# Kernel tuning notes

Measured on AMD Instinct MI355X. Metric: run time of the kernel, lower is better.

## Reference

```python
import jax, jax.numpy as jnp
import numpy as np

NEG_BIG = -9e15
ALPHA = 0.2  # leakyrelu negative slope

N, F_IN, F_OUT = 8192, 512, 64


def setup_inputs() -> dict:
    key = jax.random.key(0)
    k1, k2, k3, k4 = jax.random.split(key, 4)
    input = jax.random.normal(k1, (N, F_IN), dtype=jnp.float32)
    adj = jax.random.randint(k2, (N, N), 0, 2, dtype=jnp.int32)
    W = jax.random.normal(k3, (F_IN, F_OUT), dtype=jnp.float32) * 0.05
    a = jax.random.normal(k4, (2 * F_OUT, 1), dtype=jnp.float32) * 0.1
    return {"input": input, "adj": adj, "W": W, "a": a}


def reference(input, adj, W, a):
    # h: [N, F_out]
    h = input @ W
    # The original builds a_input[i,j] = concat(h_i, h_j) and dots with a.
    # Decompose: e_ij = leakyrelu(h_i @ a_src + h_j @ a_dst) -- identical math,
    # avoids the N*N*2F intermediate.
    a_src = a[:F_OUT, 0]  # [F_out]
    a_dst = a[F_OUT:, 0]  # [F_out]
    s_src = h @ a_src     # [N]
    s_dst = h @ a_dst     # [N]
    e = jax.nn.leaky_relu(s_src[:, None] + s_dst[None, :], negative_slope=ALPHA)  # [N, N]
    masked = jnp.where(adj > 0, e, jnp.float32(NEG_BIG))
    attention = jax.nn.softmax(masked, axis=1)  # dropout omitted (eval mode)
    h_prime = attention @ h  # [N, F_out]
    return jax.nn.elu(h_prime)  # concat=True
```

## Files before the change

kernel.cpp:

```cpp
#include <hip/hip_runtime.h>
#include <hip/hip_bf16.h>

namespace {
constexpr int kN    = 8192;
constexpr int kFin  = 512;
constexpr int kFout = 64;
constexpr float kAlpha = 0.2f;
constexpr int kJSplit = 4;
constexpr int kJLen   = kN / kJSplit;
constexpr int kChunks = kJLen / 128;

using bf16x8 = __attribute__((ext_vector_type(8))) short;
using f32x4  = __attribute__((ext_vector_type(4))) float;

__device__ __forceinline__ unsigned short f2bf(float x) {
  return __builtin_bit_cast(unsigned short, __float2bfloat16(x));
}
__device__ __forceinline__ float lrelu(float x) {
  return fmaxf(x, kAlpha * x);
}
__device__ __forceinline__ unsigned int fkey(float x) {
  unsigned int b = __float_as_uint(x);
  return (b & 0x80000000u) ? ~b : (b | 0x80000000u);
}
__device__ __forceinline__ float fdec(unsigned int k) {
  return (k & 0x80000000u) ? __uint_as_float(k ^ 0x80000000u) : __uint_as_float(~k);
}
}

__global__ __launch_bounds__(256) void k_prep(
    const int* __restrict__ adj, const float* __restrict__ X,
    const float* __restrict__ W, const float* __restrict__ A,
    unsigned long long* __restrict__ mask, unsigned short* __restrict__ hTf,
    float* __restrict__ s_src, float* __restrict__ s_dst,
    unsigned int* __restrict__ Smax_u)
{
  const int t = threadIdx.x;
  const int wv = t >> 6, lane = t & 63;

  if (blockIdx.x >= 512) {
    const int mwave = (blockIdx.x - 512) * 4 + wv;
    constexpr int kMaskWaves = 2048 * 4;
    const int4* __restrict__ a4 = (const int4*)adj;
    const int grp = lane >> 4;
    const unsigned long long shft = 4ull * (lane & 15);
#pragma unroll 2
    for (int it = 0; it < 32; ++it) {
      const size_t base4 = ((size_t)it * kMaskWaves + mwave) * 64;
      const int4 v = a4[base4 + lane];
      const unsigned int nib = (v.x > 0 ? 1u : 0u) | (v.y > 0 ? 2u : 0u) |
                               (v.z > 0 ? 4u : 0u) | (v.w > 0 ? 8u : 0u);
      unsigned long long val = (unsigned long long)nib << shft;
      val |= __shfl_xor(val, 1, 64);
      val |= __shfl_xor(val, 2, 64);
      val |= __shfl_xor(val, 4, 64);
      val |= __shfl_xor(val, 8, 64);
      if ((lane & 15) == 0) {
        const size_t baseInt = base4 * 4;
        const size_t row = baseInt >> 13;
        const size_t jw  = (baseInt & 8191) >> 6;
        mask[row * 128 + jw + grp] = val;
      }
    }
    return;
  }

  const int wvu = __builtin_amdgcn_readfirstlane(wv);
  const int f = lane;
  const int i0 = blockIdx.x * 16;
  const int r0l = wvu * 4;

  __shared__ unsigned short h_sm[16][64];
  __shared__ float red[4];

  const float* x0 = X + (size_t)(i0 + r0l) * kFin;
  float acc0 = 0.f, acc1 = 0.f, acc2 = 0.f, acc3 = 0.f;
#pragma unroll 2
  for (int k = 0; k < kFin; k += 4) {
    const float4 xa = *(const float4*)(x0 + k);
    const float4 xb = *(const float4*)(x0 + kFin + k);
    const float4 xc = *(const float4*)(x0 + 2 * kFin + k);
    const float4 xd = *(const float4*)(x0 + 3 * kFin + k);
#pragma unroll
    for (int j = 0; j < 4; ++j) {
      const float wk = W[(k + j) * kFout + f];
      acc0 = fmaf(((const float*)&xa)[j], wk, acc0);
      acc1 = fmaf(((const float*)&xb)[j], wk, acc1);
      acc2 = fmaf(((const float*)&xc)[j], wk, acc2);
      acc3 = fmaf(((const float*)&xd)[j], wk, acc3);
    }
  }

  const float asrc = A[f], adst = A[kFout + f];
  float accs[4] = {acc0, acc1, acc2, acc3};
  float dmax = -3.4e38f;
#pragma unroll
  for (int r = 0; r < 4; ++r) {
    float vs = accs[r] * asrc;
    float vd = accs[r] * adst;
#pragma unroll
    for (int off = 32; off > 0; off >>= 1) {
      vs += __shfl_xor(vs, off, 64);
      vd += __shfl_xor(vd, off, 64);
    }
    if (f == 0) {
      s_src[i0 + r0l + r] = vs;
      s_dst[i0 + r0l + r] = vd;
      dmax = fmaxf(dmax, vd);
    }
    h_sm[r0l + r][f] = f2bf(accs[r]);
  }
  if (f == 0) red[wvu] = dmax;
  __syncthreads();
  if (t == 0) {
    float m = fmaxf(fmaxf(red[0], red[1]), fmaxf(red[2], red[3]));
    atomicMax(Smax_u, fkey(m));
  }

  if (t < 128) {
    const int jblk = i0 >> 5, half = (i0 >> 4) & 1;
    const int w = t >> 5, li = t & 31;
    const int ln = half * 32 + li;
    const int ql = li >> 4, fcol = w * 16 + (li & 15);
    bf16x8 v;
#pragma unroll
    for (int e = 0; e < 8; ++e) v[e] = (short)h_sm[ql * 8 + e][fcol];
    *(bf16x8*)(hTf + (size_t)jblk * 2048 + w * 512 + (size_t)ln * 8) = v;
  }
}

__global__ __launch_bounds__(256) void k_attn(
    const unsigned long long* __restrict__ mask,
    const unsigned short* __restrict__ hTf,
    const float* __restrict__ s_src, const float* __restrict__ s_dst,
    const unsigned int* __restrict__ Smax_u, float* __restrict__ accp,
    float* __restrict__ lp)
{
  const int t = threadIdx.x;
  const int wv = t >> 6, lane = t & 63;
  const int b = blockIdx.x;
  const int i0 = (b >> 2) * 16;
  const int q = b & 3;
  const int jbase = q * kJLen;
  const int mrow = lane & 15, quad = lane >> 4;

  __shared__ float Racc[4][16][64];
  __shared__ float Rl[4][16];

  const float S = fdec(*Smax_u);
  const float ssrc = s_src[i0 + mrow];
  const float mr = lrelu(ssrc + S);

  float l_acc = 0.f;
  f32x4 acc0 = {0.f,0.f,0.f,0.f}, acc1 = {0.f,0.f,0.f,0.f};
  f32x4 acc2 = {0.f,0.f,0.f,0.f}, acc3 = {0.f,0.f,0.f,0.f};

  const unsigned long long* mptr =
      mask + (size_t)(i0 + mrow) * 128 + (jbase >> 6) + (wv >> 1);
  const int sh = (wv & 1) * 32 + quad * 8;
  const float4* dptr = (const float4*)(s_dst + jbase + wv * 32 + quad * 8);
  const unsigned short* hbase =
      hTf + ((size_t)(jbase >> 5) + wv) * 2048 + (size_t)lane * 8;

  unsigned long long m0 = mptr[0], m1 = mptr[2], m2 = mptr[4], m3 = mptr[6];
  float4 D0a = dptr[0],  D1a = dptr[1];
  float4 D0b = dptr[32], D1b = dptr[33];

  auto phase = [&](int c, unsigned long long mw, float4& D0, float4& D1)
      __attribute__((always_inline)) {
    const unsigned short* hc = hbase + (size_t)c * 8192;
    const uint4 hv0 = *(const uint4*)(hc + 0 * 512);
    const uint4 hv1 = *(const uint4*)(hc + 1 * 512);
    const uint4 hv2 = *(const uint4*)(hc + 2 * 512);
    const uint4 hv3 = *(const uint4*)(hc + 3 * 512);

    const unsigned int B = (unsigned int)(mw >> sh) & 0xffu;
    float pv[8];
    {
      const float* dd = (const float*)&D0;
#pragma unroll
      for (int j = 0; j < 4; ++j) {
        const float e = lrelu(ssrc + dd[j]);
        pv[j] = (B >> j) & 1u ? __expf(e - mr) : 0.f;
      }
      dd = (const float*)&D1;
#pragma unroll
      for (int j = 0; j < 4; ++j) {
        const float e = lrelu(ssrc + dd[j]);
        pv[4 + j] = (B >> (4 + j)) & 1u ? __expf(e - mr) : 0.f;
      }
    }
    bf16x8 ps;
#pragma unroll
    for (int j = 0; j < 8; ++j) {
      l_acc += pv[j];
      ps[j] = (short)f2bf(pv[j]);
    }

    if (c + 2 < kChunks) {
      D0 = dptr[(c + 2) * 32]; D1 = dptr[(c + 2) * 32 + 1];
    }

    acc0 = __builtin_amdgcn_mfma_f32_16x16x32_bf16(ps, __builtin_bit_cast(bf16x8, hv0), acc0, 0, 0, 0);
    acc1 = __builtin_amdgcn_mfma_f32_16x16x32_bf16(ps, __builtin_bit_cast(bf16x8, hv1), acc1, 0, 0, 0);
    acc2 = __builtin_amdgcn_mfma_f32_16x16x32_bf16(ps, __builtin_bit_cast(bf16x8, hv2), acc2, 0, 0, 0);
    acc3 = __builtin_amdgcn_mfma_f32_16x16x32_bf16(ps, __builtin_bit_cast(bf16x8, hv3), acc3, 0, 0, 0);
  };

  for (int g = 0; g < 4; ++g) {
    unsigned long long n0 = 0, n1 = 0, n2 = 0, n3 = 0;
    if (g < 3) {
      n0 = mptr[g * 8 + 8]; n1 = mptr[g * 8 + 10];
      n2 = mptr[g * 8 + 12]; n3 = mptr[g * 8 + 14];
    }
    phase(g * 4 + 0, m0, D0a, D1a);
    phase(g * 4 + 1, m1, D0b, D1b);
    phase(g * 4 + 2, m2, D0a, D1a);
    phase(g * 4 + 3, m3, D0b, D1b);
    m0 = n0; m1 = n1; m2 = n2; m3 = n3;
  }

  float lv = l_acc;
  lv += __shfl_xor(lv, 16, 64);
  lv += __shfl_xor(lv, 32, 64);
  if (quad == 0) Rl[wv][mrow] = lv;

#pragma unroll
  for (int reg = 0; reg < 4; ++reg) {
    Racc[wv][quad * 4 + reg][0 * 16 + mrow] = acc0[reg];
    Racc[wv][quad * 4 + reg][1 * 16 + mrow] = acc1[reg];
    Racc[wv][quad * 4 + reg][2 * 16 + mrow] = acc2[reg];
    Racc[wv][quad * 4 + reg][3 * 16 + mrow] = acc3[reg];
  }
  __syncthreads();

  float* ab = accp + (size_t)b * 16 * 64;
  const int rr = t >> 4, ff = t & 15;
#pragma unroll
  for (int s = 0; s < 4; ++s) {
    const int fc = s * 16 + ff;
    ab[rr * 64 + fc] = Racc[0][rr][fc] + Racc[1][rr][fc] + Racc[2][rr][fc] + Racc[3][rr][fc];
  }
  if (t < 16) lp[(size_t)b * 16 + t] = Rl[0][t] + Rl[1][t] + Rl[2][t] + Rl[3][t];
}

__global__ __launch_bounds__(256) void k_comb(const float* __restrict__ accp,
                                              const float* __restrict__ lp,
                                              float* __restrict__ out)
{
  const int gid = blockIdx.x * 256 + threadIdx.x;
  const int i = gid >> 6, f = gid & 63;
  const int ib = i >> 4, il = i & 15;
  const int b0 = ib * kJSplit;
  float a = 0.f, l = 0.f;
#pragma unroll
  for (int qq = 0; qq < kJSplit; ++qq) {
    a += accp[((size_t)(b0 + qq) * 16 + il) * 64 + f];
    l += lp[(size_t)(b0 + qq) * 16 + il];
  }
  float v = a / l;
  v = v > 0.f ? v : __expf(v) - 1.f;
  out[gid] = v;
}

extern "C" void kernel_launch(void* const* d_in, const int* in_sizes, int n_in,
                              void* d_out, int out_size, void* d_ws, size_t ws_size,
                              hipStream_t stream) {
  const float* X   = (const float*)d_in[0];
  const int*   adj = (const int*)d_in[1];
  const float* W   = (const float*)d_in[2];
  const float* A   = (const float*)d_in[3];
  float* out = (float*)d_out;

  char* ws = (char*)d_ws;
  unsigned long long* mask = (unsigned long long*)ws;  ws += (size_t)kN * 128 * 8;
  unsigned short* hTf = (unsigned short*)ws;  ws += (size_t)kN * kFout * 2;
  float* s_src = (float*)ws;                  ws += kN * 4;
  float* s_dst = (float*)ws;                  ws += kN * 4;
  unsigned int* Smax_u = (unsigned int*)ws;   ws += 256;
  float* accp  = (float*)ws;                  ws += (size_t)(kN / 16) * kJSplit * 16 * 64 * 4;
  float* lp    = (float*)ws;

  hipMemsetAsync(Smax_u, 0, 4, stream);
  k_prep <<<512 + 2048, 256, 0, stream>>>(adj, X, W, A, mask, hTf, s_src, s_dst, Smax_u);
  k_attn <<<(kN / 16) * kJSplit, 256, 0, stream>>>(mask, hTf, s_src, s_dst, Smax_u, accp, lp);
  k_comb <<<kN * kFout / 256, 256, 0, stream>>>(accp, lp, out);
}
```

Measured before the change: 427.0 us.

## Process 32 rows per attention block to reuse h loads across two MFMA tiles

```diff
diff --git a/kernel.cpp b/kernel.cpp
--- a/kernel.cpp
+++ b/kernel.cpp
@@ -38,15 +38,14 @@
   const int t = threadIdx.x;
   const int wv = t >> 6, lane = t & 63;
 
-  if (blockIdx.x >= 512) {
-    const int mwave = (blockIdx.x - 512) * 4 + wv;
-    constexpr int kMaskWaves = 2048 * 4;
+  if (blockIdx.x < 2048) {
+    const int mwave = blockIdx.x * 4 + wv;
     const int4* __restrict__ a4 = (const int4*)adj;
     const int grp = lane >> 4;
     const unsigned long long shft = 4ull * (lane & 15);
-#pragma unroll 2
+#pragma unroll 4
     for (int it = 0; it < 32; ++it) {
-      const size_t base4 = ((size_t)it * kMaskWaves + mwave) * 64;
+      const size_t base4 = ((size_t)it * 8192 + mwave) * 64;
       const int4 v = a4[base4 + lane];
       const unsigned int nib = (v.x > 0 ? 1u : 0u) | (v.y > 0 ? 2u : 0u) |
                                (v.z > 0 ? 4u : 0u) | (v.w > 0 ? 8u : 0u);
@@ -67,7 +66,7 @@
 
   const int wvu = __builtin_amdgcn_readfirstlane(wv);
   const int f = lane;
-  const int i0 = blockIdx.x * 16;
+  const int i0 = (blockIdx.x - 2048) * 16;
   const int r0l = wvu * 4;
 
   __shared__ unsigned short h_sm[16][64];
@@ -129,7 +128,7 @@
   }
 }
 
-__global__ __launch_bounds__(256) void k_attn(
+__global__ __launch_bounds__(256, 4) void k_attn(
     const unsigned long long* __restrict__ mask,
     const unsigned short* __restrict__ hTf,
     const float* __restrict__ s_src, const float* __restrict__ s_dst,
@@ -139,109 +138,121 @@
   const int t = threadIdx.x;
   const int wv = t >> 6, lane = t & 63;
   const int b = blockIdx.x;
-  const int i0 = (b >> 2) * 16;
-  const int q = b & 3;
-  const int jbase = q * kJLen;
+  const int i0 = (b >> 2) * 32;
+  const int jbase = (b & 3) * kJLen;
   const int mrow = lane & 15, quad = lane >> 4;
 
-  __shared__ float Racc[4][16][64];
-  __shared__ float Rl[4][16];
+  __shared__ float Racc[4][32][64];
+  __shared__ float Rl[4][32];
 
   const float S = fdec(*Smax_u);
-  const float ssrc = s_src[i0 + mrow];
-  const float mr = lrelu(ssrc + S);
-
-  float l_acc = 0.f;
-  f32x4 acc0 = {0.f,0.f,0.f,0.f}, acc1 = {0.f,0.f,0.f,0.f};
-  f32x4 acc2 = {0.f,0.f,0.f,0.f}, acc3 = {0.f,0.f,0.f,0.f};
-
-  const unsigned long long* mptr =
+  const float ssA = s_src[i0 + mrow];
+  const float ssB = s_src[i0 + 16 + mrow];
+  const float mrA = lrelu(ssA + S);
+  const float mrB = lrelu(ssB + S);
+
+  float lA = 0.f, lB = 0.f;
+  f32x4 aA0 = {0,0,0,0}, aA1 = {0,0,0,0}, aA2 = {0,0,0,0}, aA3 = {0,0,0,0};
+  f32x4 aB0 = {0,0,0,0}, aB1 = {0,0,0,0}, aB2 = {0,0,0,0}, aB3 = {0,0,0,0};
+
+  const unsigned long long* mptrA =
       mask + (size_t)(i0 + mrow) * 128 + (jbase >> 6) + (wv >> 1);
+  const unsigned long long* mptrB = mptrA + 16 * 128;
   const int sh = (wv & 1) * 32 + quad * 8;
   const float4* dptr = (const float4*)(s_dst + jbase + wv * 32 + quad * 8);
   const unsigned short* hbase =
       hTf + ((size_t)(jbase >> 5) + wv) * 2048 + (size_t)lane * 8;
 
-  unsigned long long m0 = mptr[0], m1 = mptr[2], m2 = mptr[4], m3 = mptr[6];
+  unsigned long long MAa = mptrA[0], MBa = mptrB[0];
+  unsigned long long MAb = mptrA[2], MBb = mptrB[2];
   float4 D0a = dptr[0],  D1a = dptr[1];
   float4 D0b = dptr[32], D1b = dptr[33];
 
-  auto phase = [&](int c, unsigned long long mw, float4& D0, float4& D1)
-      __attribute__((always_inline)) {
+  auto phase = [&](int c, unsigned long long& MA, unsigned long long& MB,
+                   float4& D0, float4& D1) __attribute__((always_inline)) {
     const unsigned short* hc = hbase + (size_t)c * 8192;
     const uint4 hv0 = *(const uint4*)(hc + 0 * 512);
     const uint4 hv1 = *(const uint4*)(hc + 1 * 512);
     const uint4 hv2 = *(const uint4*)(hc + 2 * 512);
     const uint4 hv3 = *(const uint4*)(hc + 3 * 512);
 
-    const unsigned int B = (unsigned int)(mw >> sh) & 0xffu;
-    float pv[8];
-    {
-      const float* dd = (const float*)&D0;
-#pragma unroll
-      for (int j = 0; j < 4; ++j) {
-        const float e = lrelu(ssrc + dd[j]);
-        pv[j] = (B >> j) & 1u ? __expf(e - mr) : 0.f;
-      }
-      dd = (const float*)&D1;
-#pragma unroll
-      for (int j = 0; j < 4; ++j) {
-        const float e = lrelu(ssrc + dd[j]);
-        pv[4 + j] = (B >> (4 + j)) & 1u ? __expf(e - mr) : 0.f;
-      }
-    }
-    bf16x8 ps;
+    const unsigned int BA = (unsigned int)(MA >> sh) & 0xffu;
+    const unsigned int BB = (unsigned int)(MB >> sh) & 0xffu;
+    float pvA[8], pvB[8];
+    const float* dd0 = (const float*)&D0;
+    const float* dd1 = (const float*)&D1;
+#pragma unroll
+    for (int j = 0; j < 4; ++j) {
+      const float d = dd0[j];
+      const float eA = lrelu(ssA + d);
+      const float eB = lrelu(ssB + d);
+      pvA[j] = (BA >> j) & 1u ? __expf(eA - mrA) : 0.f;
+      pvB[j] = (BB >> j) & 1u ? __expf(eB - mrB) : 0.f;
+    }
+#pragma unroll
+    for (int j = 0; j < 4; ++j) {
+      const float d = dd1[j];
+      const float eA = lrelu(ssA + d);
+      const float eB = lrelu(ssB + d);
+      pvA[4 + j] = (BA >> (4 + j)) & 1u ? __expf(eA - mrA) : 0.f;
+      pvB[4 + j] = (BB >> (4 + j)) & 1u ? __expf(eB - mrB) : 0.f;
+    }
+    bf16x8 psA, psB;
 #pragma unroll
     for (int j = 0; j < 8; ++j) {
-      l_acc += pv[j];
-      ps[j] = (short)f2bf(pv[j]);
+      lA += pvA[j];  lB += pvB[j];
+      psA[j] = (short)f2bf(pvA[j]);
+      psB[j] = (short)f2bf(pvB[j]);
     }
 
     if (c + 2 < kChunks) {
+      MA = mptrA[(c + 2) * 2]; MB = mptrB[(c + 2) * 2];
       D0 = dptr[(c + 2) * 32]; D1 = dptr[(c + 2) * 32 + 1];
     }
 
-    acc0 = __builtin_amdgcn_mfma_f32_16x16x32_bf16(ps, __builtin_bit_cast(bf16x8, hv0), acc0, 0, 0, 0);
-    acc1 = __builtin_amdgcn_mfma_f32_16x16x32_bf16(ps, __builtin_bit_cast(bf16x8, hv1), acc1, 0, 0, 0);
-    acc2 = __builtin_amdgcn_mfma_f32_16x16x32_bf16(ps, __builtin_bit_cast(bf16x8, hv2), acc2, 0, 0, 0);
-    acc3 = __builtin_amdgcn_mfma_f32_16x16x32_bf16(ps, __builtin_bit_cast(bf16x8, hv3), acc3, 0, 0, 0);
+    aA0 = __builtin_amdgcn_mfma_f32_16x16x32_bf16(psA, __builtin_bit_cast(bf16x8, hv0), aA0, 0, 0, 0);
+    aB0 = __builtin_amdgcn_mfma_f32_16x16x32_bf16(psB, __builtin_bit_cast(bf16x8, hv0), aB0, 0, 0, 0);
+    aA1 = __builtin_amdgcn_mfma_f32_16x16x32_bf16(psA, __builtin_bit_cast(bf16x8, hv1), aA1, 0, 0, 0);
+    aB1 = __builtin_amdgcn_mfma_f32_16x16x32_bf16(psB, __builtin_bit_cast(bf16x8, hv1), aB1, 0, 0, 0);
+    aA2 = __builtin_amdgcn_mfma_f32_16x16x32_bf16(psA, __builtin_bit_cast(bf16x8, hv2), aA2, 0, 0, 0);
+    aB2 = __builtin_amdgcn_mfma_f32_16x16x32_bf16(psB, __builtin_bit_cast(bf16x8, hv2), aB2, 0, 0, 0);
+    aA3 = __builtin_amdgcn_mfma_f32_16x16x32_bf16(psA, __builtin_bit_cast(bf16x8, hv3), aA3, 0, 0, 0);
+    aB3 = __builtin_amdgcn_mfma_f32_16x16x32_bf16(psB, __builtin_bit_cast(bf16x8, hv3), aB3, 0, 0, 0);
   };
 
-  for (int g = 0; g < 4; ++g) {
-    unsigned long long n0 = 0, n1 = 0, n2 = 0, n3 = 0;
-    if (g < 3) {
-      n0 = mptr[g * 8 + 8]; n1 = mptr[g * 8 + 10];
-      n2 = mptr[g * 8 + 12]; n3 = mptr[g * 8 + 14];
-    }
-    phase(g * 4 + 0, m0, D0a, D1a);
-    phase(g * 4 + 1, m1, D0b, D1b);
-    phase(g * 4 + 2, m2, D0a, D1a);
-    phase(g * 4 + 3, m3, D0b, D1b);
-    m0 = n0; m1 = n1; m2 = n2; m3 = n3;
-  }
-
-  float lv = l_acc;
-  lv += __shfl_xor(lv, 16, 64);
-  lv += __shfl_xor(lv, 32, 64);
-  if (quad == 0) Rl[wv][mrow] = lv;
+  for (int c = 0; c < kChunks; c += 2) {
+    phase(c,     MAa, MBa, D0a, D1a);
+    phase(c + 1, MAb, MBb, D0b, D1b);
+  }
+
+  lA += __shfl_xor(lA, 16, 64);
+  lA += __shfl_xor(lA, 32, 64);
+  lB += __shfl_xor(lB, 16, 64);
+  lB += __shfl_xor(lB, 32, 64);
+  if (quad == 0) { Rl[wv][mrow] = lA; Rl[wv][16 + mrow] = lB; }
 
 #pragma unroll
   for (int reg = 0; reg < 4; ++reg) {
-    Racc[wv][quad * 4 + reg][0 * 16 + mrow] = acc0[reg];
-    Racc[wv][quad * 4 + reg][1 * 16 + mrow] = acc1[reg];
-    Racc[wv][quad * 4 + reg][2 * 16 + mrow] = acc2[reg];
-    Racc[wv][quad * 4 + reg][3 * 16 + mrow] = acc3[reg];
+    const int rA = quad * 4 + reg, rB = 16 + quad * 4 + reg;
+    Racc[wv][rA][ 0 + mrow] = aA0[reg];
+    Racc[wv][rA][16 + mrow] = aA1[reg];
+    Racc[wv][rA][32 + mrow] = aA2[reg];
+    Racc[wv][rA][48 + mrow] = aA3[reg];
+    Racc[wv][rB][ 0 + mrow] = aB0[reg];
+    Racc[wv][rB][16 + mrow] = aB1[reg];
+    Racc[wv][rB][32 + mrow] = aB2[reg];
+    Racc[wv][rB][48 + mrow] = aB3[reg];
   }
   __syncthreads();
 
-  float* ab = accp + (size_t)b * 16 * 64;
-  const int rr = t >> 4, ff = t & 15;
-#pragma unroll
-  for (int s = 0; s < 4; ++s) {
-    const int fc = s * 16 + ff;
-    ab[rr * 64 + fc] = Racc[0][rr][fc] + Racc[1][rr][fc] + Racc[2][rr][fc] + Racc[3][rr][fc];
-  }
-  if (t < 16) lp[(size_t)b * 16 + t] = Rl[0][t] + Rl[1][t] + Rl[2][t] + Rl[3][t];
+  float* ab = accp + (size_t)b * 32 * 64;
+#pragma unroll
+  for (int s = 0; s < 8; ++s) {
+    const int idx = s * 256 + t;
+    const int r = idx >> 6, f = idx & 63;
+    ab[idx] = Racc[0][r][f] + Racc[1][r][f] + Racc[2][r][f] + Racc[3][r][f];
+  }
+  if (t < 32) lp[(size_t)b * 32 + t] = Rl[0][t] + Rl[1][t] + Rl[2][t] + Rl[3][t];
 }
 
 __global__ __launch_bounds__(256) void k_comb(const float* __restrict__ accp,
@@ -250,13 +261,13 @@
 {
   const int gid = blockIdx.x * 256 + threadIdx.x;
   const int i = gid >> 6, f = gid & 63;
-  const int ib = i >> 4, il = i & 15;
+  const int ib = i >> 5, il = i & 31;
   const int b0 = ib * kJSplit;
   float a = 0.f, l = 0.f;
 #pragma unroll
   for (int qq = 0; qq < kJSplit; ++qq) {
-    a += accp[((size_t)(b0 + qq) * 16 + il) * 64 + f];
-    l += lp[(size_t)(b0 + qq) * 16 + il];
+    a += accp[((size_t)(b0 + qq) * 32 + il) * 64 + f];
+    l += lp[(size_t)(b0 + qq) * 32 + il];
   }
   float v = a / l;
   v = v > 0.f ? v : __expf(v) - 1.f;
@@ -278,11 +289,11 @@
   float* s_src = (float*)ws;                  ws += kN * 4;
   float* s_dst = (float*)ws;                  ws += kN * 4;
   unsigned int* Smax_u = (unsigned int*)ws;   ws += 256;
-  float* accp  = (float*)ws;                  ws += (size_t)(kN / 16) * kJSplit * 16 * 64 * 4;
+  float* accp  = (float*)ws;                  ws += (size_t)1024 * 32 * 64 * 4;
   float* lp    = (float*)ws;
 
   hipMemsetAsync(Smax_u, 0, 4, stream);
-  k_prep <<<512 + 2048, 256, 0, stream>>>(adj, X, W, A, mask, hTf, s_src, s_dst, Smax_u);
-  k_attn <<<(kN / 16) * kJSplit, 256, 0, stream>>>(mask, hTf, s_src, s_dst, Smax_u, accp, lp);
+  k_prep <<<2048 + 512, 256, 0, stream>>>(adj, X, W, A, mask, hTf, s_src, s_dst, Smax_u);
+  k_attn <<<1024, 256, 0, stream>>>(mask, hTf, s_src, s_dst, Smax_u, accp, lp);
   k_comb <<<kN * kFout / 256, 256, 0, stream>>>(accp, lp, out);
 }
```

After: 449.6 us. 5.3% more time.
